# Performance work log

Measured on AMD Instinct MI355X. Metric: run time of the kernel, lower is better.

The kernel has to match this reference:

```python
import jax, jax.numpy as jnp
import numpy as np

N_NODES = 50000
N_EDGES = 800000
F_IN = 32
HID = 64
K = 4  # Chebyshev order in GConvLSTM(node_features, hidden, 4)


def setup_inputs() -> dict:
    key = jax.random.key(0)
    ks = jax.random.split(key, 14)
    x = jax.random.normal(ks[0], (N_NODES, F_IN), dtype=jnp.float32)
    edge_index = jax.random.randint(ks[1], (2, N_EDGES), 0, N_NODES, dtype=jnp.int64)
    edge_weight = jax.random.uniform(ks[2], (N_EDGES,), dtype=jnp.float32)
    s = 0.05
    # gate order: i, f, c, o
    Wx = jax.random.normal(ks[3], (4, K, F_IN, HID), dtype=jnp.float32) * s  # ChebConv weights on x
    bx = jax.random.normal(ks[4], (4, HID), dtype=jnp.float32) * s          # ChebConv biases on x
    Wh = jax.random.normal(ks[5], (4, K, HID, HID), dtype=jnp.float32) * s  # ChebConv weights on h
    bh = jax.random.normal(ks[6], (4, HID), dtype=jnp.float32) * s          # ChebConv biases on h
    wc = jax.random.normal(ks[7], (3, HID), dtype=jnp.float32) * s          # peephole w_c_i, w_c_f, w_c_o
    bg = jax.random.normal(ks[8], (4, HID), dtype=jnp.float32) * s          # gate biases b_i, b_f, b_c, b_o
    lin_w = jax.random.normal(ks[9], (HID, 1), dtype=jnp.float32) * s
    lin_b = jax.random.normal(ks[10], (1,), dtype=jnp.float32) * s
    return {"x": x, "edge_index": edge_index, "edge_weight": edge_weight,
            "Wx": Wx, "bx": bx, "Wh": Wh, "bh": bh, "wc": wc, "bg": bg,
            "lin_w": lin_w, "lin_b": lin_b}


def _cheb_norm(edge_index, edge_weight, num_nodes):
    # ChebConv.__norm__, sym normalization, lambda_max=2.0:
    # L_hat off-diagonal = -D^{-1/2} A D^{-1/2}, diagonal = 0.
    src, dst = edge_index[0], edge_index[1]
    deg = jax.ops.segment_sum(edge_weight, src, num_segments=num_nodes)
    d_inv_sqrt = jnp.where(deg > 0, jax.lax.rsqrt(jnp.maximum(deg, 1e-30)), 0.0)
    norm = -d_inv_sqrt[src] * edge_weight * d_inv_sqrt[dst]
    return src, dst, norm


def _cheb_conv(v, src, dst, norm, W, b, num_nodes):
    # ChebConv forward: out = sum_k T_k(L_hat) v @ W[k] + b, with propagate
    # = segment_sum of norm * v[src] at dst.
    def prop(t):
        return jax.ops.segment_sum(norm[:, None] * t[src], dst, num_segments=num_nodes)
    Tx0 = v
    out = Tx0 @ W[0]
    Tx1 = prop(Tx0)
    out = out + Tx1 @ W[1]
    for k in range(2, W.shape[0]):
        Tx2 = 2.0 * prop(Tx1) - Tx0
        out = out + Tx2 @ W[k]
        Tx0, Tx1 = Tx1, Tx2
    return out + b


def reference(x, edge_index, edge_weight, Wx, bx, Wh, bh, wc, bg, lin_w, lin_b):
    N = x.shape[0]
    src, dst, norm = _cheb_norm(edge_index, edge_weight, N)
    H = jnp.zeros((N, Wh.shape[-1]), dtype=x.dtype)
    C = jnp.zeros((N, Wh.shape[-1]), dtype=x.dtype)

    def gate(g, v_state):
        return (_cheb_conv(x, src, dst, norm, Wx[g], bx[g], N)
                + _cheb_conv(v_state, src, dst, norm, Wh[g], bh[g], N))

    I = jax.nn.sigmoid(gate(0, H) + wc[0] * C + bg[0])
    F = jax.nn.sigmoid(gate(1, H) + wc[1] * C + bg[1])
    T = jnp.tanh(gate(2, H) + bg[2])
    C = F * C + I * T
    O = jax.nn.sigmoid(gate(3, H) + wc[2] * C + bg[3])
    H = O * jnp.tanh(C)
    # dropout(p=0.25) is identity at inference; linear head HID -> 1
    return H @ lin_w + lin_b
```

## Files before the change

### kernel.cpp

```cpp
#include <hip/hip_runtime.h>
#include <math.h>


#define NT 256
#define RSH 16384
#define RSF 16384
#define NCH 32

typedef __attribute__((ext_vector_type(8))) short short8v;
typedef __attribute__((ext_vector_type(8))) unsigned short ushort8v;
typedef __attribute__((ext_vector_type(4))) float f32x4;

__device__ __forceinline__ short f2bf(float f) {
    unsigned u = __float_as_uint(f);
    u += 0x7FFFu + ((u >> 16) & 1u);
    return (short)(u >> 16);
}
__device__ __forceinline__ float bf2f(unsigned short b) {
    return __uint_as_float((unsigned)b << 16);
}

__global__ __launch_bounds__(1024)
void k_hist(const int* __restrict__ src, const int* __restrict__ dst,
            const float* __restrict__ w, float* __restrict__ degPart,
            int* __restrict__ cntPart, int nE, int N) {
    __shared__ float s_deg[RSH];
    __shared__ int   s_cnt[RSH];
    const int r = blockIdx.x / NCH, b = blockIdx.x % NCH;
    const int base = r * RSH;
    for (int i = threadIdx.x; i < RSH; i += 1024) { s_deg[i] = 0.f; s_cnt[i] = 0; }
    __syncthreads();
    const int chunk = (nE + NCH - 1) / NCH;
    const int e0 = b * chunk, e1 = min(e0 + chunk, nE);
    for (int e = e0 + (int)threadIdx.x; e < e1; e += 1024) {
        int s = src[e], d = dst[e];
        unsigned so = (unsigned)(s - base), dof = (unsigned)(d - base);
        if (so < RSH) atomicAdd(&s_deg[so], w[e]);
        if (dof < RSH) atomicAdd(&s_cnt[dof], 1);
    }
    __syncthreads();
    const int lim = min(RSH, N - base);
    for (int i = threadIdx.x; i < lim; i += 1024) {
        degPart[(size_t)b * N + base + i] = s_deg[i];
        cntPart[(size_t)b * N + base + i] = s_cnt[i];
    }
}

__global__ __launch_bounds__(NT)
void k_reduce_scanA(const float* __restrict__ degPart, const int* __restrict__ cntPart,
                    float* __restrict__ dinv, int* __restrict__ cnt,
                    int* __restrict__ rowptr, int* __restrict__ partials, int N) {
    __shared__ int s[NT];
    int t = threadIdx.x, i = blockIdx.x * NT + t;
    int c = 0;
    if (i < N) {
        float d = 0.f;
#pragma unroll
        for (int b = 0; b < NCH; ++b) {
            d += degPart[(size_t)b * N + i];
            c += cntPart[(size_t)b * N + i];
        }
        dinv[i] = d > 0.f ? rsqrtf(d) : 0.f;
        cnt[i] = c;
    }
    s[t] = c;
    __syncthreads();
    for (int off = 1; off < NT; off <<= 1) {
        int u = (t >= off) ? s[t - off] : 0;
        __syncthreads();
        s[t] += u;
        __syncthreads();
    }
    if (i < N) rowptr[i] = s[t] - c;
    if (t == NT - 1) partials[blockIdx.x] = s[t];
}

__global__ void k_scanB(int* __restrict__ partials, int nb) {
    __shared__ int s[1024];
    int t = threadIdx.x;
    int v = (t < nb) ? partials[t] : 0;
    s[t] = v;
    __syncthreads();
    for (int off = 1; off < 1024; off <<= 1) {
        int u = (t >= off) ? s[t - off] : 0;
        __syncthreads();
        s[t] += u;
        __syncthreads();
    }
    if (t < nb) partials[t] = s[t] - v;
}

__global__ void k_scanC_off(int* __restrict__ rowptr, const int* __restrict__ partials,
                            int* __restrict__ cntPart, int N) {
    int n = blockIdx.x * NT + threadIdx.x;
    if (n >= N) return;
    int v = rowptr[n] + partials[blockIdx.x];
    rowptr[n] = v;
    int s = v;
#pragma unroll
    for (int b = 0; b < NCH; ++b) {
        int t = cntPart[(size_t)b * N + n];
        cntPart[(size_t)b * N + n] = s;
        s += t;
    }
}

__global__ __launch_bounds__(1024)
void k_fill2(const int* __restrict__ src, const int* __restrict__ dst,
             const float* __restrict__ w, const float* __restrict__ dinv,
             const int* __restrict__ offs, int2* __restrict__ entries,
             int nE, int N) {
    __shared__ int s_cur[RSF];
    const int r = blockIdx.x / NCH, b = blockIdx.x % NCH;
    const int base = r * RSF;
    const int lim = min(RSF, N - base);
    for (int i = threadIdx.x; i < lim; i += 1024)
        s_cur[i] = offs[(size_t)b * N + base + i];
    __syncthreads();
    const int chunk = (nE + NCH - 1) / NCH;
    const int e0 = b * chunk, e1 = min(e0 + chunk, nE);
    for (int e = e0 + (int)threadIdx.x; e < e1; e += 1024) {
        int d = dst[e];
        unsigned dof = (unsigned)(d - base);
        if (dof < RSF) {
            int s = src[e];
            float nv = -dinv[s] * w[e] * dinv[d];
            int pos = atomicAdd(&s_cur[dof], 1);
            entries[pos] = make_int2(s, __float_as_int(nv));
        }
    }
}

__device__ __forceinline__ void bf8_fma(float* acc, ushort8v v, float s) {
#pragma unroll
    for (int j = 0; j < 8; ++j)
        acc[j] = fmaf(s, bf2f(v[j]), acc[j]);
}

__global__ __launch_bounds__(256)
void k_gather_bf(const unsigned short* __restrict__ tb,
                 const unsigned short* __restrict__ subb,
                 short* __restrict__ outb,
                 const int* __restrict__ rowptr, const int* __restrict__ cnt,
                 const int2* __restrict__ entries, float scale, int N) {
    int idx = blockIdx.x * blockDim.x + threadIdx.x;
    if (idx >= N * 8) return;
    int n = idx >> 3, tq = idx & 3, half = (idx >> 2) & 1;
    int beg = rowptr[n], end = beg + cnt[n];
    float acc0[8] = {0, 0, 0, 0, 0, 0, 0, 0};
    float acc1[8] = {0, 0, 0, 0, 0, 0, 0, 0};
    int i = beg + half;
    for (; i + 6 < end; i += 8) {
        int2 e0 = entries[i];
        int2 e1 = entries[i + 2];
        int2 e2 = entries[i + 4];
        int2 e3 = entries[i + 6];
        ushort8v v0 = *reinterpret_cast<const ushort8v*>(tb + (size_t)e0.x * 32 + tq * 8);
        ushort8v v1 = *reinterpret_cast<const ushort8v*>(tb + (size_t)e1.x * 32 + tq * 8);
        ushort8v v2 = *reinterpret_cast<const ushort8v*>(tb + (size_t)e2.x * 32 + tq * 8);
        ushort8v v3 = *reinterpret_cast<const ushort8v*>(tb + (size_t)e3.x * 32 + tq * 8);
        bf8_fma(acc0, v0, __int_as_float(e0.y));
        bf8_fma(acc1, v1, __int_as_float(e1.y));
        bf8_fma(acc0, v2, __int_as_float(e2.y));
        bf8_fma(acc1, v3, __int_as_float(e3.y));
    }
    for (; i < end; i += 2) {
        int2 e0 = entries[i];
        ushort8v v0 = *reinterpret_cast<const ushort8v*>(tb + (size_t)e0.x * 32 + tq * 8);
        bf8_fma(acc0, v0, __int_as_float(e0.y));
    }
    float r[8];
#pragma unroll
    for (int j = 0; j < 8; ++j) {
        r[j] = acc0[j] + acc1[j];
        r[j] += __shfl_xor(r[j], 4);
    }
    if (!half) {
        if (subb) {
            ushort8v sv = *reinterpret_cast<const ushort8v*>(subb + (size_t)n * 32 + tq * 8);
#pragma unroll
            for (int j = 0; j < 8; ++j) r[j] = fmaf(scale, r[j], -bf2f(sv[j]));
        } else {
#pragma unroll
            for (int j = 0; j < 8; ++j) r[j] *= scale;
        }
        short8v rb;
#pragma unroll
        for (int j = 0; j < 8; ++j) rb[j] = f2bf(r[j]);
        *reinterpret_cast<short8v*>(outb + (size_t)n * 32 + tq * 8) = rb;
    }
}

__global__ void k_prepack_xb(const float* __restrict__ Wx, short* __restrict__ P,
                             const float* __restrict__ x, short* __restrict__ xb,
                             int n4) {
    int idx = blockIdx.x * blockDim.x + threadIdx.x;
    if (idx < 12 * 4 * 64) {
        int lane = idx & 63;
        int kt = (idx >> 6) & 3;
        int nt = idx >> 8;
        int gate = (nt < 4) ? 0 : (nt < 8) ? 2 : 3;
        int h = (nt & 3) * 16 + (lane & 15);
        int fb = (lane >> 4) * 8;
        short8v v;
#pragma unroll
        for (int j = 0; j < 8; ++j)
            v[j] = f2bf(Wx[((size_t)(gate * 4 + kt) * 32 + fb + j) * 64 + h]);
        *(reinterpret_cast<short8v*>(P) + idx) = v;
        return;
    }
    int i = idx - 12 * 4 * 64;
    if (i >= n4) return;
    const float4 v = *reinterpret_cast<const float4*>(x + (size_t)i * 4);
    short4 rb;
    rb.x = f2bf(v.x); rb.y = f2bf(v.y); rb.z = f2bf(v.z); rb.w = f2bf(v.w);
    *reinterpret_cast<short4*>(xb + (size_t)i * 4) = rb;
}

__device__ __forceinline__ float sigf(float x) {
    return __builtin_amdgcn_rcpf(1.f + __builtin_amdgcn_exp2f(-1.4426950408889634f * x));
}
__device__ __forceinline__ float tanhf_fast(float x) {
    float e = __builtin_amdgcn_exp2f(2.8853900817779268f * x);
    return 1.f - 2.f * __builtin_amdgcn_rcpf(e + 1.f);
}

__global__ __launch_bounds__(256)
void k_final_g3(const short* __restrict__ xb, const short* __restrict__ t1b,
                const unsigned short* __restrict__ t2b,
                const short* __restrict__ P,
                const int* __restrict__ rowptr, const int* __restrict__ cnt,
                const int2* __restrict__ entries,
                const float* __restrict__ bx, const float* __restrict__ bh,
                const float* __restrict__ wc, const float* __restrict__ bg,
                const float* __restrict__ lin_w, const float* __restrict__ lin_b,
                float* __restrict__ out, int N) {
    const int wave = threadIdx.x >> 6, lane = threadIdx.x & 63;
    const int nb = blockIdx.x * 64 + wave * 16;
    const int rc = min(nb + (lane & 15), N - 1);
    const int ko = (lane >> 4) * 8;

    int beg = rowptr[rc], end = beg + cnt[rc];
    float acc0[8] = {0, 0, 0, 0, 0, 0, 0, 0};
    float acc1[8] = {0, 0, 0, 0, 0, 0, 0, 0};
    int i = beg;
    for (; i + 3 < end; i += 4) {
        int2 e0 = entries[i];
        int2 e1 = entries[i + 1];
        int2 e2 = entries[i + 2];
        int2 e3 = entries[i + 3];
        ushort8v v0 = *reinterpret_cast<const ushort8v*>(t2b + (size_t)e0.x * 32 + ko);
        ushort8v v1 = *reinterpret_cast<const ushort8v*>(t2b + (size_t)e1.x * 32 + ko);
        ushort8v v2 = *reinterpret_cast<const ushort8v*>(t2b + (size_t)e2.x * 32 + ko);
        ushort8v v3 = *reinterpret_cast<const ushort8v*>(t2b + (size_t)e3.x * 32 + ko);
        bf8_fma(acc0, v0, __int_as_float(e0.y));
        bf8_fma(acc1, v1, __int_as_float(e1.y));
        bf8_fma(acc0, v2, __int_as_float(e2.y));
        bf8_fma(acc1, v3, __int_as_float(e3.y));
    }
    for (; i < end; ++i) {
        int2 e0 = entries[i];
        ushort8v v0 = *reinterpret_cast<const ushort8v*>(t2b + (size_t)e0.x * 32 + ko);
        bf8_fma(acc0, v0, __int_as_float(e0.y));
    }

    short8v A0 = *reinterpret_cast<const short8v*>(xb  + (size_t)rc * 32 + ko);
    short8v A1 = *reinterpret_cast<const short8v*>(t1b + (size_t)rc * 32 + ko);
    short8v A2 = *reinterpret_cast<const short8v*>(
        reinterpret_cast<const short*>(t2b) + (size_t)rc * 32 + ko);
    short8v A3;
#pragma unroll
    for (int j = 0; j < 8; ++j)
        A3[j] = f2bf(2.f * (acc0[j] + acc1[j]) - bf2f((unsigned short)A1[j]));

    const short8v* Pv = reinterpret_cast<const short8v*>(P);
    f32x4 acc[12];
#pragma unroll
    for (int nt = 0; nt < 12; ++nt) {
        const short8v* Pb = Pv + (size_t)nt * 4 * 64 + lane;
        f32x4 a = {0.f, 0.f, 0.f, 0.f};
        a = __builtin_amdgcn_mfma_f32_16x16x32_bf16(A0, Pb[0],   a, 0, 0, 0);
        a = __builtin_amdgcn_mfma_f32_16x16x32_bf16(A1, Pb[64],  a, 0, 0, 0);
        a = __builtin_amdgcn_mfma_f32_16x16x32_bf16(A2, Pb[128], a, 0, 0, 0);
        a = __builtin_amdgcn_mfma_f32_16x16x32_bf16(A3, Pb[192], a, 0, 0, 0);
        acc[nt] = a;
    }

    const int hq = lane & 15;
    const int ng = lane >> 4;
    const float lb = lin_b[0];
    float p[4] = {0.f, 0.f, 0.f, 0.f};
#pragma unroll
    for (int ht = 0; ht < 4; ++ht) {
        int h = ht * 16 + hq;
        float bI = bx[h] + bh[h] + bg[h];
        float bC = bx[128 + h] + bh[128 + h] + bg[128 + h];
        float bO = bx[192 + h] + bh[192 + h] + bg[192 + h];
        float w2 = wc[128 + h];
        float lw = lin_w[h];
#pragma unroll
        for (int r = 0; r < 4; ++r) {
            float I = sigf(acc[ht][r] + bI);
            float T = tanhf_fast(acc[4 + ht][r] + bC);
            float C = I * T;
            float O = sigf(acc[8 + ht][r] + bO + w2 * C);
            float H = O * tanhf_fast(C);
            p[r] = fmaf(H, lw, p[r]);
        }
    }
#pragma unroll
    for (int r = 0; r < 4; ++r) {
        float v = p[r];
        v += __shfl_xor(v, 1);
        v += __shfl_xor(v, 2);
        v += __shfl_xor(v, 4);
        v += __shfl_xor(v, 8);
        if (hq == 0) {
            int n = nb + ng * 4 + r;
            if (n < N) out[n] = v + lb;
        }
    }
}

extern "C" void kernel_launch(void* const* d_in, const int* in_sizes, int n_in,
                              void* d_out, int out_size, void* d_ws, size_t ws_size,
                              hipStream_t stream) {
    const float* x   = (const float*)d_in[0];
    const int*   ei  = (const int*)d_in[1];
    const float* ew  = (const float*)d_in[2];
    const float* Wx  = (const float*)d_in[3];
    const float* bx  = (const float*)d_in[4];
    const float* bh  = (const float*)d_in[6];
    const float* wcp = (const float*)d_in[7];
    const float* bg  = (const float*)d_in[8];
    const float* lw  = (const float*)d_in[9];
    const float* lb  = (const float*)d_in[10];
    float* out = (float*)d_out;

    const int N  = in_sizes[0] / 32;
    const int nE = in_sizes[2];
    const int* src = ei;
    const int* dst = ei + nE;

    char* ws = (char*)d_ws;
    size_t off = 0;
    float* dinv    = (float*)(ws + off); off += (size_t)N * 4;
    int*   cnt     = (int*)(ws + off);   off += (size_t)N * 4;
    int*   rowptr  = (int*)(ws + off);   off += (size_t)N * 4;
    int*   partials= (int*)(ws + off);   off += 1024 * 4;
    short* P       = (short*)(ws + off); off += 12 * 4 * 64 * 8 * 2;
    int2*  entries = (int2*)(ws + off);  off += (size_t)nE * 8;
    float* degPart = (float*)(ws + off); off += (size_t)NCH * N * 4;
    int*   cntPart = (int*)(ws + off);   off += (size_t)NCH * N * 4;
    short* xbuf    = (short*)(ws + off); off += (size_t)N * 32 * 2;
    short* Tx1b    = (short*)(ws + off); off += (size_t)N * 32 * 2;
    short* Tx2b    = (short*)(ws + off); off += (size_t)N * 32 * 2;

    const int nb = (N + NT - 1) / NT;
    const int nRangeH = (N + RSH - 1) / RSH;
    const int nRangeF = (N + RSF - 1) / RSF;

    k_hist<<<nRangeH * NCH, 1024, 0, stream>>>(src, dst, ew, degPart, cntPart, nE, N);
    k_prepack_xb<<<(12 * 4 * 64 + N * 8 + NT - 1) / NT, NT, 0, stream>>>(Wx, P, x, xbuf, N * 8);
    k_reduce_scanA<<<nb, NT, 0, stream>>>(degPart, cntPart, dinv, cnt, rowptr,
                                          partials, N);
    k_scanB<<<1, 1024, 0, stream>>>(partials, nb);
    k_scanC_off<<<nb, NT, 0, stream>>>(rowptr, partials, cntPart, N);
    k_fill2<<<nRangeF * NCH, 1024, 0, stream>>>(src, dst, ew, dinv, cntPart,
                                                entries, nE, N);

    const int gb = (N * 8 + NT - 1) / NT;
    k_gather_bf<<<gb, NT, 0, stream>>>((const unsigned short*)xbuf, nullptr,
                                       Tx1b, rowptr, cnt, entries, 1.f, N);
    k_gather_bf<<<gb, NT, 0, stream>>>((const unsigned short*)Tx1b,
                                       (const unsigned short*)xbuf,
                                       Tx2b, rowptr, cnt, entries, 2.f, N);

    const int fb = (N + 63) / 64;
    k_final_g3<<<fb, NT, 0, stream>>>(xbuf, Tx1b, (const unsigned short*)Tx2b, P,
                                      rowptr, cnt, entries, bx, bh, wcp, bg,
                                      lw, lb, out, N);
}
```

Measured before the change: 118.3 us.

## Fuse histogram with prepack, pack counts to 16-bit, merge scan kernels

The degree/count histogram and the weight/x bf16 prepack become one launch, with prepack blocks appended after the histogram blocks. Per-chunk destination counts are stored as packed 16-bit values in both LDS and global memory, which halves count traffic; the chunk count doubles and the LDS range widens. The two scan-fixup kernels merge into one that recomputes each block prefix by reducing the partials, and each thread now handles two nodes. Per-chunk offsets reuse the degree-partials buffer. The cost is more LDS per histogram block and counts capped at 16 bits per chunk.

```diff
diff --git a/kernel.cpp b/kernel.cpp
--- a/kernel.cpp
+++ b/kernel.cpp
@@ -3,9 +3,9 @@
 
 
 #define NT 256
-#define RSH 16384
+#define NCH 64
+#define RSH 20480
 #define RSF 16384
-#define NCH 32
 
 typedef __attribute__((ext_vector_type(8))) short short8v;
 typedef __attribute__((ext_vector_type(8))) unsigned short ushort8v;
@@ -21,14 +21,43 @@
 }
 
 __global__ __launch_bounds__(1024)
-void k_hist(const int* __restrict__ src, const int* __restrict__ dst,
-            const float* __restrict__ w, float* __restrict__ degPart,
-            int* __restrict__ cntPart, int nE, int N) {
-    __shared__ float s_deg[RSH];
-    __shared__ int   s_cnt[RSH];
-    const int r = blockIdx.x / NCH, b = blockIdx.x % NCH;
+void k_front(const int* __restrict__ src, const int* __restrict__ dst,
+             const float* __restrict__ w, float* __restrict__ degPart,
+             unsigned short* __restrict__ cntPart,
+             const float* __restrict__ Wx, short* __restrict__ P,
+             const float* __restrict__ x, short* __restrict__ xb,
+             int nE, int N, int histB, int n4) {
+    __shared__ float    s_deg[RSH];
+    __shared__ unsigned s_cnt2[RSH / 2];
+    const int bid = blockIdx.x;
+    if (bid >= histB) {
+        int idx = (bid - histB) * 1024 + (int)threadIdx.x;
+        if (idx < 12 * 4 * 64) {
+            int lane = idx & 63;
+            int kt = (idx >> 6) & 3;
+            int nt = idx >> 8;
+            int gate = (nt < 4) ? 0 : (nt < 8) ? 2 : 3;
+            int h = (nt & 3) * 16 + (lane & 15);
+            int fb = (lane >> 4) * 8;
+            short8v v;
+#pragma unroll
+            for (int j = 0; j < 8; ++j)
+                v[j] = f2bf(Wx[((size_t)(gate * 4 + kt) * 32 + fb + j) * 64 + h]);
+            *(reinterpret_cast<short8v*>(P) + idx) = v;
+            return;
+        }
+        int i = idx - 12 * 4 * 64;
+        if (i >= n4) return;
+        const float4 v = *reinterpret_cast<const float4*>(x + (size_t)i * 4);
+        short4 rb;
+        rb.x = f2bf(v.x); rb.y = f2bf(v.y); rb.z = f2bf(v.z); rb.w = f2bf(v.w);
+        *reinterpret_cast<short4*>(xb + (size_t)i * 4) = rb;
+        return;
+    }
+    const int r = bid / NCH, b = bid % NCH;
     const int base = r * RSH;
-    for (int i = threadIdx.x; i < RSH; i += 1024) { s_deg[i] = 0.f; s_cnt[i] = 0; }
+    for (int i = threadIdx.x; i < RSH; i += 1024) s_deg[i] = 0.f;
+    for (int i = threadIdx.x; i < RSH / 2; i += 1024) s_cnt2[i] = 0u;
     __syncthreads();
     const int chunk = (nE + NCH - 1) / NCH;
     const int e0 = b * chunk, e1 = min(e0 + chunk, nE);
@@ -36,34 +65,47 @@
         int s = src[e], d = dst[e];
         unsigned so = (unsigned)(s - base), dof = (unsigned)(d - base);
         if (so < RSH) atomicAdd(&s_deg[so], w[e]);
-        if (dof < RSH) atomicAdd(&s_cnt[dof], 1);
+        if (dof < RSH) atomicAdd(&s_cnt2[dof >> 1], 1u << ((dof & 1) * 16));
     }
     __syncthreads();
     const int lim = min(RSH, N - base);
-    for (int i = threadIdx.x; i < lim; i += 1024) {
+    for (int i = threadIdx.x; i < lim; i += 1024)
         degPart[(size_t)b * N + base + i] = s_deg[i];
-        cntPart[(size_t)b * N + base + i] = s_cnt[i];
-    }
+    unsigned* cp32 = reinterpret_cast<unsigned*>(cntPart + (size_t)b * N + base);
+    const int pairs = lim >> 1;
+    for (int i = threadIdx.x; i < pairs; i += 1024) cp32[i] = s_cnt2[i];
+    if ((lim & 1) && threadIdx.x == 0)
+        cntPart[(size_t)b * N + base + lim - 1] =
+            (unsigned short)(s_cnt2[lim >> 1] & 0xFFFFu);
 }
 
 __global__ __launch_bounds__(NT)
-void k_reduce_scanA(const float* __restrict__ degPart, const int* __restrict__ cntPart,
+void k_reduce_scanA(const float* __restrict__ degPart,
+                    const unsigned short* __restrict__ cntPart,
                     float* __restrict__ dinv, int* __restrict__ cnt,
                     int* __restrict__ rowptr, int* __restrict__ partials, int N) {
     __shared__ int s[NT];
-    int t = threadIdx.x, i = blockIdx.x * NT + t;
-    int c = 0;
-    if (i < N) {
-        float d = 0.f;
-#pragma unroll
+    const int t = threadIdx.x;
+    const int n0 = blockIdx.x * (NT * 2) + t * 2;
+    float d0 = 0.f, d1 = 0.f;
+    int c0 = 0, c1 = 0;
+    if (n0 < N) {
+#pragma unroll 8
         for (int b = 0; b < NCH; ++b) {
-            d += degPart[(size_t)b * N + i];
-            c += cntPart[(size_t)b * N + i];
-        }
-        dinv[i] = d > 0.f ? rsqrtf(d) : 0.f;
-        cnt[i] = c;
-    }
-    s[t] = c;
+            const float2 dv = *reinterpret_cast<const float2*>(degPart + (size_t)b * N + n0);
+            d0 += dv.x; d1 += dv.y;
+            unsigned cc = *reinterpret_cast<const unsigned*>(cntPart + (size_t)b * N + n0);
+            c0 += (int)(cc & 0xFFFFu); c1 += (int)(cc >> 16);
+        }
+        dinv[n0] = d0 > 0.f ? rsqrtf(d0) : 0.f;
+        cnt[n0] = c0;
+        if (n0 + 1 < N) {
+            dinv[n0 + 1] = d1 > 0.f ? rsqrtf(d1) : 0.f;
+            cnt[n0 + 1] = c1;
+        } else c1 = 0;
+    }
+    int cs = c0 + c1;
+    s[t] = cs;
     __syncthreads();
     for (int off = 1; off < NT; off <<= 1) {
         int u = (t >= off) ? s[t - off] : 0;
@@ -71,37 +113,45 @@
         s[t] += u;
         __syncthreads();
     }
-    if (i < N) rowptr[i] = s[t] - c;
+    int ex = s[t] - cs;
+    if (n0 < N) {
+        rowptr[n0] = ex;
+        if (n0 + 1 < N) rowptr[n0 + 1] = ex + c0;
+    }
     if (t == NT - 1) partials[blockIdx.x] = s[t];
 }
 
-__global__ void k_scanB(int* __restrict__ partials, int nb) {
-    __shared__ int s[1024];
-    int t = threadIdx.x;
-    int v = (t < nb) ? partials[t] : 0;
-    s[t] = v;
+__global__ __launch_bounds__(NT)
+void k_scan_off(int* __restrict__ rowptr, const int* __restrict__ partials, int nb2,
+                const unsigned short* __restrict__ cntPart, int* __restrict__ offs,
+                int N) {
+    __shared__ int sp[NT];
+    const int t = threadIdx.x;
+    int v = (t < (int)blockIdx.x && t < nb2) ? partials[t] : 0;
+    sp[t] = v;
     __syncthreads();
-    for (int off = 1; off < 1024; off <<= 1) {
-        int u = (t >= off) ? s[t - off] : 0;
+    for (int off = NT / 2; off > 0; off >>= 1) {
+        if (t < off) sp[t] += sp[t + off];
         __syncthreads();
-        s[t] += u;
-        __syncthreads();
-    }
-    if (t < nb) partials[t] = s[t] - v;
-}
-
-__global__ void k_scanC_off(int* __restrict__ rowptr, const int* __restrict__ partials,
-                            int* __restrict__ cntPart, int N) {
-    int n = blockIdx.x * NT + threadIdx.x;
-    if (n >= N) return;
-    int v = rowptr[n] + partials[blockIdx.x];
-    rowptr[n] = v;
-    int s = v;
-#pragma unroll
+    }
+    const int prefix = sp[0];
+    const int n0 = blockIdx.x * (NT * 2) + t * 2;
+    if (n0 >= N) return;
+    const bool has1 = (n0 + 1) < N;
+    int s0 = rowptr[n0] + prefix;
+    int s1 = has1 ? rowptr[n0 + 1] + prefix : 0;
+    rowptr[n0] = s0;
+    if (has1) rowptr[n0 + 1] = s1;
+#pragma unroll 8
     for (int b = 0; b < NCH; ++b) {
-        int t = cntPart[(size_t)b * N + n];
-        cntPart[(size_t)b * N + n] = s;
-        s += t;
+        unsigned cc = *reinterpret_cast<const unsigned*>(cntPart + (size_t)b * N + n0);
+        if (has1) {
+            *reinterpret_cast<int2*>(offs + (size_t)b * N + n0) = make_int2(s0, s1);
+        } else {
+            offs[(size_t)b * N + n0] = s0;
+        }
+        s0 += (int)(cc & 0xFFFFu);
+        s1 += (int)(cc >> 16);
     }
 }
 
@@ -191,32 +241,6 @@
     }
 }
 
-__global__ void k_prepack_xb(const float* __restrict__ Wx, short* __restrict__ P,
-                             const float* __restrict__ x, short* __restrict__ xb,
-                             int n4) {
-    int idx = blockIdx.x * blockDim.x + threadIdx.x;
-    if (idx < 12 * 4 * 64) {
-        int lane = idx & 63;
-        int kt = (idx >> 6) & 3;
-        int nt = idx >> 8;
-        int gate = (nt < 4) ? 0 : (nt < 8) ? 2 : 3;
-        int h = (nt & 3) * 16 + (lane & 15);
-        int fb = (lane >> 4) * 8;
-        short8v v;
-#pragma unroll
-        for (int j = 0; j < 8; ++j)
-            v[j] = f2bf(Wx[((size_t)(gate * 4 + kt) * 32 + fb + j) * 64 + h]);
-        *(reinterpret_cast<short8v*>(P) + idx) = v;
-        return;
-    }
-    int i = idx - 12 * 4 * 64;
-    if (i >= n4) return;
-    const float4 v = *reinterpret_cast<const float4*>(x + (size_t)i * 4);
-    short4 rb;
-    rb.x = f2bf(v.x); rb.y = f2bf(v.y); rb.z = f2bf(v.z); rb.w = f2bf(v.w);
-    *reinterpret_cast<short4*>(xb + (size_t)i * 4) = rb;
-}
-
 __device__ __forceinline__ float sigf(float x) {
     return __builtin_amdgcn_rcpf(1.f + __builtin_amdgcn_exp2f(-1.4426950408889634f * x));
 }
@@ -351,22 +375,26 @@
     short* P       = (short*)(ws + off); off += 12 * 4 * 64 * 8 * 2;
     int2*  entries = (int2*)(ws + off);  off += (size_t)nE * 8;
     float* degPart = (float*)(ws + off); off += (size_t)NCH * N * 4;
-    int*   cntPart = (int*)(ws + off);   off += (size_t)NCH * N * 4;
+    unsigned short* cntPart = (unsigned short*)(ws + off); off += (size_t)NCH * N * 2;
     short* xbuf    = (short*)(ws + off); off += (size_t)N * 32 * 2;
     short* Tx1b    = (short*)(ws + off); off += (size_t)N * 32 * 2;
     short* Tx2b    = (short*)(ws + off); off += (size_t)N * 32 * 2;
 
-    const int nb = (N + NT - 1) / NT;
+    int* offs = (int*)degPart;
+
     const int nRangeH = (N + RSH - 1) / RSH;
     const int nRangeF = (N + RSF - 1) / RSF;
-
-    k_hist<<<nRangeH * NCH, 1024, 0, stream>>>(src, dst, ew, degPart, cntPart, nE, N);
-    k_prepack_xb<<<(12 * 4 * 64 + N * 8 + NT - 1) / NT, NT, 0, stream>>>(Wx, P, x, xbuf, N * 8);
-    k_reduce_scanA<<<nb, NT, 0, stream>>>(degPart, cntPart, dinv, cnt, rowptr,
-                                          partials, N);
-    k_scanB<<<1, 1024, 0, stream>>>(partials, nb);
-    k_scanC_off<<<nb, NT, 0, stream>>>(rowptr, partials, cntPart, N);
-    k_fill2<<<nRangeF * NCH, 1024, 0, stream>>>(src, dst, ew, dinv, cntPart,
+    const int histB = nRangeH * NCH;
+    const int n4 = N * 8;
+    const int xbB = (12 * 4 * 64 + n4 + 1023) / 1024;
+    const int nb2 = (N + NT * 2 - 1) / (NT * 2);
+
+    k_front<<<histB + xbB, 1024, 0, stream>>>(src, dst, ew, degPart, cntPart,
+                                              Wx, P, x, xbuf, nE, N, histB, n4);
+    k_reduce_scanA<<<nb2, NT, 0, stream>>>(degPart, cntPart, dinv, cnt, rowptr,
+                                           partials, N);
+    k_scan_off<<<nb2, NT, 0, stream>>>(rowptr, partials, nb2, cntPart, offs, N);
+    k_fill2<<<nRangeF * NCH, 1024, 0, stream>>>(src, dst, ew, dinv, offs,
                                                 entries, nE, N);
 
     const int gb = (N * 8 + NT - 1) / NT;
```

Measured after the change: 103.4 us. 1.14x faster.
